# Optimization experiments

Measured on AMD Instinct MI355X. Metric: run time of the kernel, lower is better.

## Reference

```python
import jax, jax.numpy as jnp
import numpy as np

N_NODES = 50000
N_EDGES = 800000
IN_C, HID_C, OUT_C = 128, 64, 40


def setup_inputs() -> dict:
    key = jax.random.key(0)
    ks = jax.random.split(key, 8)
    x = jax.random.normal(ks[0], (N_NODES, IN_C), dtype=jnp.float32)
    edge_index = jax.random.randint(ks[1], (2, N_EDGES), 0, N_NODES, dtype=jnp.int32)
    # Glorot-style init for the three GCNConv linear layers (bias zero as in PyG default reset)
    def glorot(k, fan_in, fan_out):
        lim = jnp.sqrt(6.0 / (fan_in + fan_out)).astype(jnp.float32)
        return jax.random.uniform(k, (fan_in, fan_out), dtype=jnp.float32, minval=-lim, maxval=lim)
    return {
        "x": x,
        "edge_index": edge_index,
        "W1": glorot(ks[2], IN_C, HID_C), "b1": jnp.zeros((HID_C,), jnp.float32),
        "W2": glorot(ks[3], HID_C, HID_C), "b2": jnp.zeros((HID_C,), jnp.float32),
        "W3": glorot(ks[4], HID_C, OUT_C), "b3": jnp.zeros((OUT_C,), jnp.float32),
    }


def _gcn_norm(edge_index, num_nodes):
    # PyG gcn_norm: add self-loops (weight 1), symmetric D^-1/2 (A+I) D^-1/2.
    loop = jnp.arange(num_nodes, dtype=edge_index.dtype)
    row = jnp.concatenate([edge_index[0], loop])  # source
    col = jnp.concatenate([edge_index[1], loop])  # target
    w = jnp.ones(row.shape[0], dtype=jnp.float32)
    deg = jax.ops.segment_sum(w, col, num_segments=num_nodes)
    dinv = jnp.where(deg > 0, jax.lax.rsqrt(deg), 0.0)
    norm = dinv[row] * w * dinv[col]  # [E+N]
    return row, col, norm


def _gcn_conv(x, row, col, norm, W, b):
    h = x @ W                         # linear first, as in PyG GCNConv
    msg = h[row] * norm[:, None]      # gather + scale  [E+N, F]
    agg = jax.ops.segment_sum(msg, col, num_segments=x.shape[0])
    return agg + b


def reference(x, edge_index, W1, b1, W2, b2, W3, b3):
    row, col, norm = _gcn_norm(edge_index, x.shape[0])
    h = jax.nn.relu(_gcn_conv(x, row, col, norm, W1, b1))   # dropout: eval-mode identity
    h = jax.nn.relu(_gcn_conv(h, row, col, norm, W2, b2))
    h = _gcn_conv(h, row, col, norm, W3, b3)
    return jax.nn.log_softmax(h, axis=-1)
```

## Files before the change

### kernel.cpp

```cpp
#include <hip/hip_runtime.h>
#include <hip/hip_bf16.h>
#include <math.h>


#define BSHIFT 10
#define CHUNK 2048
#define CAP 24576

__global__ __launch_bounds__(64) void tinyzero_kernel(int* __restrict__ p) {
  p[threadIdx.x] = 0;
}


__global__ __launch_bounds__(256) void bucketA_kernel(const int* __restrict__ row,
                                                      const int* __restrict__ col,
                                                      int* __restrict__ bcursor,
                                                      int2* __restrict__ tmp, int e) {
  __shared__ int bcnt[64], bstart[64], bbase[64];
  __shared__ int2 stage[CHUNK];
  int tid = threadIdx.x;
  int base = blockIdx.x * CHUNK;
  int cnt = e - base;
  if (cnt > CHUNK) cnt = CHUNK;
  if (tid < 64) bcnt[tid] = 0;
  __syncthreads();

  int2 ed[CHUNK / 256];
  int rk[CHUNK / 256];
#pragma unroll
  for (int k = 0; k < CHUNK / 256; ++k) {
    int j = tid + k * 256;
    if (j < cnt) {
      int c = col[base + j], r = row[base + j];
      ed[k] = make_int2(c, r);
      rk[k] = atomicAdd(&bcnt[c >> BSHIFT], 1);
    }
  }
  __syncthreads();
  if (tid < 64) {
    int v = bcnt[tid];
    int run = v;
#pragma unroll
    for (int off = 1; off < 64; off <<= 1) {
      int t = __shfl_up(run, off);
      if (tid >= off) run += t;
    }
    bstart[tid] = run - v;
    if (v > 0) bbase[tid] = atomicAdd(&bcursor[tid], v);
  }
  __syncthreads();
#pragma unroll
  for (int k = 0; k < CHUNK / 256; ++k) {
    int j = tid + k * 256;
    if (j < cnt) stage[bstart[ed[k].x >> BSHIFT] + rk[k]] = ed[k];
  }
  __syncthreads();
  for (int s = tid; s < cnt; s += 256) {
    int2 ev = stage[s];
    int b = ev.x >> BSHIFT;
    tmp[(size_t)b * CAP + bbase[b] + (s - bstart[b])] = ev;
  }
}


__global__ __launch_bounds__(256) void scatterB_kernel(const int2* __restrict__ tmp,
                                                       const int* __restrict__ bcursor,
                                                       int4* __restrict__ meta,
                                                       float* __restrict__ dinv,
                                                       int* __restrict__ csr, int n) {
  __shared__ int cnt[1 << BSHIFT];
  __shared__ int part[256];
  int tid = threadIdx.x;
  int b = blockIdx.x;
  int node0 = b << BSHIFT;
  int m = bcursor[b];
  const int2* src = tmp + (size_t)b * CAP;

  for (int t = tid; t < (1 << BSHIFT); t += 256) cnt[t] = 0;
  __syncthreads();
  for (int i = tid; i < m; i += 256)
    atomicAdd(&cnt[src[i].x & ((1 << BSHIFT) - 1)], 1);
  __syncthreads();

  int c0 = cnt[tid * 4 + 0], c1 = cnt[tid * 4 + 1];
  int c2 = cnt[tid * 4 + 2], c3 = cnt[tid * 4 + 3];
  int lsum = c0 + c1 + c2 + c3;
  part[tid] = lsum;
  __syncthreads();
#pragma unroll
  for (int off = 1; off < 256; off <<= 1) {
    int t = (tid >= off) ? part[tid - off] : 0;
    __syncthreads();
    part[tid] += t;
    __syncthreads();
  }
  int e0 = (tid == 0 ? 0 : part[tid - 1]);
  int e1 = e0 + c0, e2 = e1 + c1, e3 = e2 + c2;
  int base = b * CAP;

  int nd = node0 + tid * 4;
  if (nd + 0 < n) { float d = rsqrtf((float)(c0 + 1)); meta[nd + 0] = make_int4(base + e0, c0, __float_as_int(d), 0); dinv[nd + 0] = d; }
  if (nd + 1 < n) { float d = rsqrtf((float)(c1 + 1)); meta[nd + 1] = make_int4(base + e1, c1, __float_as_int(d), 0); dinv[nd + 1] = d; }
  if (nd + 2 < n) { float d = rsqrtf((float)(c2 + 1)); meta[nd + 2] = make_int4(base + e2, c2, __float_as_int(d), 0); dinv[nd + 2] = d; }
  if (nd + 3 < n) { float d = rsqrtf((float)(c3 + 1)); meta[nd + 3] = make_int4(base + e3, c3, __float_as_int(d), 0); dinv[nd + 3] = d; }
  __syncthreads();
  cnt[tid * 4 + 0] = e0; cnt[tid * 4 + 1] = e1;
  cnt[tid * 4 + 2] = e2; cnt[tid * 4 + 3] = e3;
  __syncthreads();

  for (int i = tid; i < m; i += 256) {
    int2 ev = src[i];
    int pos = atomicAdd(&cnt[ev.x & ((1 << BSHIFT) - 1)], 1);
    csr[base + pos] = ev.y;
  }
}


template <int K, int F>
__global__ __launch_bounds__(256) void gemm_kernel(const float* __restrict__ X,
                                                   const float* __restrict__ W,
                                                   const float* __restrict__ dinv,
                                                   __hip_bfloat16* __restrict__ Y, int n) {
  __shared__ float xs[16][K];
  int tid = threadIdx.x;
  int node0 = blockIdx.x * 16;
  constexpr int KV = K / 4;
  const float4* X4 = (const float4*)X;
  for (int i = tid; i < 16 * KV; i += 256) {
    int r = i / KV, c = i % KV;
    int nd = node0 + r;
    float4 v = make_float4(0.f, 0.f, 0.f, 0.f);
    if (nd < n) v = X4[(size_t)nd * KV + c];
    ((float4*)&xs[r][0])[c] = v;
  }
  __syncthreads();
  int g = tid >> 6, lane = tid & 63;
  if (lane < F) {
    float acc0 = 0.f, acc1 = 0.f, acc2 = 0.f, acc3 = 0.f;
#pragma unroll 8
    for (int k = 0; k < K; ++k) {
      float w = W[k * F + lane];
      acc0 += xs[g * 4 + 0][k] * w;
      acc1 += xs[g * 4 + 1][k] * w;
      acc2 += xs[g * 4 + 2][k] * w;
      acc3 += xs[g * 4 + 3][k] * w;
    }
    float accs[4] = {acc0, acc1, acc2, acc3};
#pragma unroll
    for (int j = 0; j < 4; ++j) {
      int nd = node0 + g * 4 + j;
      if (nd < n) Y[(size_t)nd * F + lane] = __float2bfloat16(accs[j] * dinv[nd]);
    }
  }
}


__device__ __forceinline__ float bflo(unsigned int u) {
  return __uint_as_float(u << 16);
}
__device__ __forceinline__ float bfhi(unsigned int u) {
  return __uint_as_float(u & 0xffff0000u);
}

template <int F, int MODE>
__global__ __launch_bounds__(256) void agg_kernel(const unsigned short* __restrict__ Hs,
                                                  const int* __restrict__ csr,
                                                  const int4* __restrict__ meta,
                                                  const float* __restrict__ bias,
                                                  float* __restrict__ Y, int n) {
  constexpr int FO = F / 8;
  int wv = (blockIdx.x * 256 + threadIdx.x) >> 6;
  int lane = threadIdx.x & 63;
  int q = lane >> 4;
  int l16 = lane & 15;
  int sub = l16 >> 3;
  int fid = lane & 7;
  int node = wv * 4 + q;
  if (node >= n) return;
  bool activeF = (FO == 8) || (fid < FO);
  int qbase = q * 16;

  int4 mt = meta[node];
  int s = mt.x, e = mt.x + mt.y;
  float di = __int_as_float(mt.z);

  float a0 = 0.f, a1 = 0.f, a2 = 0.f, a3 = 0.f;
  float a4 = 0.f, a5 = 0.f, a6 = 0.f, a7 = 0.f;
  if (sub == 0 && activeF) {
    uint4 u = *(const uint4*)(Hs + (size_t)node * F + 8 * fid);
    a0 = bflo(u.x); a1 = bfhi(u.x); a2 = bflo(u.y); a3 = bfhi(u.y);
    a4 = bflo(u.z); a5 = bfhi(u.z); a6 = bflo(u.w); a7 = bfhi(u.w);
  }

  for (int base = s; base < e; base += 16) {
    int rem = e - base;
    int cnt = rem < 16 ? rem : 16;
    int p = csr[base + (l16 < cnt ? l16 : 0)];
    int j = 0;
    for (; j + 8 <= cnt; j += 8) {
      int r0 = __shfl(p, qbase + j + 0 + sub);
      int r1 = __shfl(p, qbase + j + 2 + sub);
      int r2 = __shfl(p, qbase + j + 4 + sub);
      int r3 = __shfl(p, qbase + j + 6 + sub);
      if (activeF) {
        uint4 u0 = *(const uint4*)(Hs + (size_t)r0 * F + 8 * fid);
        uint4 u1 = *(const uint4*)(Hs + (size_t)r1 * F + 8 * fid);
        uint4 u2 = *(const uint4*)(Hs + (size_t)r2 * F + 8 * fid);
        uint4 u3 = *(const uint4*)(Hs + (size_t)r3 * F + 8 * fid);
        a0 += bflo(u0.x); a1 += bfhi(u0.x); a2 += bflo(u0.y); a3 += bfhi(u0.y);
        a4 += bflo(u0.z); a5 += bfhi(u0.z); a6 += bflo(u0.w); a7 += bfhi(u0.w);
        a0 += bflo(u1.x); a1 += bfhi(u1.x); a2 += bflo(u1.y); a3 += bfhi(u1.y);
        a4 += bflo(u1.z); a5 += bfhi(u1.z); a6 += bflo(u1.w); a7 += bfhi(u1.w);
        a0 += bflo(u2.x); a1 += bfhi(u2.x); a2 += bflo(u2.y); a3 += bfhi(u2.y);
        a4 += bflo(u2.z); a5 += bfhi(u2.z); a6 += bflo(u2.w); a7 += bfhi(u2.w);
        a0 += bflo(u3.x); a1 += bfhi(u3.x); a2 += bflo(u3.y); a3 += bfhi(u3.y);
        a4 += bflo(u3.z); a5 += bfhi(u3.z); a6 += bflo(u3.w); a7 += bfhi(u3.w);
      }
    }
    for (; j < cnt; j += 2) {
      int idx = j + sub;
      int r = __shfl(p, qbase + (idx < cnt ? idx : j));
      if (activeF && idx < cnt) {
        uint4 u = *(const uint4*)(Hs + (size_t)r * F + 8 * fid);
        a0 += bflo(u.x); a1 += bfhi(u.x); a2 += bflo(u.y); a3 += bfhi(u.y);
        a4 += bflo(u.z); a5 += bfhi(u.z); a6 += bflo(u.w); a7 += bfhi(u.w);
      }
    }
  }

  a0 += __shfl_xor(a0, 8);
  a1 += __shfl_xor(a1, 8);
  a2 += __shfl_xor(a2, 8);
  a3 += __shfl_xor(a3, 8);
  a4 += __shfl_xor(a4, 8);
  a5 += __shfl_xor(a5, 8);
  a6 += __shfl_xor(a6, 8);
  a7 += __shfl_xor(a7, 8);

  if (MODE == 0) {
    if (sub == 0 && activeF) {
      float4 b0 = *(const float4*)(bias + 8 * fid);
      float4 b1 = *(const float4*)(bias + 8 * fid + 4);
      float v0 = a0 * di + b0.x, v1 = a1 * di + b0.y;
      float v2 = a2 * di + b0.z, v3 = a3 * di + b0.w;
      float v4 = a4 * di + b1.x, v5 = a5 * di + b1.y;
      float v6 = a6 * di + b1.z, v7 = a7 * di + b1.w;
      v0 = v0 > 0.f ? v0 : 0.f; v1 = v1 > 0.f ? v1 : 0.f;
      v2 = v2 > 0.f ? v2 : 0.f; v3 = v3 > 0.f ? v3 : 0.f;
      v4 = v4 > 0.f ? v4 : 0.f; v5 = v5 > 0.f ? v5 : 0.f;
      v6 = v6 > 0.f ? v6 : 0.f; v7 = v7 > 0.f ? v7 : 0.f;
      float* yp = Y + (size_t)node * F + 8 * fid;
      *(float4*)yp = make_float4(v0, v1, v2, v3);
      *(float4*)(yp + 4) = make_float4(v4, v5, v6, v7);
    }
  } else {
    float v0 = -INFINITY, v1 = -INFINITY, v2 = -INFINITY, v3 = -INFINITY;
    float v4 = -INFINITY, v5 = -INFINITY, v6 = -INFINITY, v7 = -INFINITY;
    if (activeF) {
      float4 b0 = *(const float4*)(bias + 8 * fid);
      float4 b1 = *(const float4*)(bias + 8 * fid + 4);
      v0 = a0 * di + b0.x; v1 = a1 * di + b0.y;
      v2 = a2 * di + b0.z; v3 = a3 * di + b0.w;
      v4 = a4 * di + b1.x; v5 = a5 * di + b1.y;
      v6 = a6 * di + b1.z; v7 = a7 * di + b1.w;
    }
    float m = fmaxf(fmaxf(fmaxf(v0, v1), fmaxf(v2, v3)),
                    fmaxf(fmaxf(v4, v5), fmaxf(v6, v7)));
#pragma unroll
    for (int off = 4; off; off >>= 1) m = fmaxf(m, __shfl_xor(m, off));
    float ex = 0.f;
    if (activeF)
      ex = expf(v0 - m) + expf(v1 - m) + expf(v2 - m) + expf(v3 - m) +
           expf(v4 - m) + expf(v5 - m) + expf(v6 - m) + expf(v7 - m);
#pragma unroll
    for (int off = 4; off; off >>= 1) ex += __shfl_xor(ex, off);
    float lg = m + logf(ex);
    if (sub == 0 && activeF) {
      float* yp = Y + (size_t)node * F + 8 * fid;
      *(float4*)yp = make_float4(v0 - lg, v1 - lg, v2 - lg, v3 - lg);
      *(float4*)(yp + 4) = make_float4(v4 - lg, v5 - lg, v6 - lg, v7 - lg);
    }
  }
}


extern "C" void kernel_launch(void* const* d_in, const int* in_sizes, int n_in,
                              void* d_out, int out_size, void* d_ws, size_t ws_size,
                              hipStream_t stream) {
  const float* x  = (const float*)d_in[0];
  const int*   ei = (const int*)d_in[1];
  const float* W1 = (const float*)d_in[2];
  const float* b1 = (const float*)d_in[3];
  const float* W2 = (const float*)d_in[4];
  const float* b2 = (const float*)d_in[5];
  const float* W3 = (const float*)d_in[6];
  const float* b3 = (const float*)d_in[7];
  float* out = (float*)d_out;

  const int N = in_sizes[0] / 128;
  const int E = in_sizes[1] / 2;
  const int* erow = ei;
  const int* ecol = ei + E;

  const int nbuckets = (N + (1 << BSHIFT) - 1) >> BSHIFT;

  auto align_up = [](size_t v) { return (v + 255) & ~(size_t)255; };
  char* ws = (char*)d_ws;
  size_t off = 0;
  int* bcursor  = (int*)(ws + off); off += align_up(64 * 4);
  int4* meta    = (int4*)(ws + off); off += align_up((size_t)N * 16);
  float* dinv   = (float*)(ws + off); off += align_up((size_t)N * 4);
  int* csr      = (int*)(ws + off); off += align_up((size_t)nbuckets * CAP * 4);
  int2* tmp     = (int2*)(ws + off); off += align_up((size_t)nbuckets * CAP * 8);
  __hip_bfloat16* bufH = (__hip_bfloat16*)(ws + off); off += align_up((size_t)N * 64 * 2);
  float* bufF   = (float*)(ws + off); off += align_up((size_t)N * 64 * 4);
  (void)ws_size;

  const int cb = (E + CHUNK - 1) / CHUNK;

  tinyzero_kernel<<<1, 64, 0, stream>>>(bcursor);
  bucketA_kernel<<<cb, 256, 0, stream>>>(erow, ecol, bcursor, tmp, E);
  scatterB_kernel<<<nbuckets, 256, 0, stream>>>(tmp, bcursor, meta, dinv, csr, N);

  const int gemm_blocks = (N + 15) / 16;
  const int agg_blocks = (N + 15) / 16;

  gemm_kernel<128, 64><<<gemm_blocks, 256, 0, stream>>>(x, W1, dinv, bufH, N);
  agg_kernel<64, 0><<<agg_blocks, 256, 0, stream>>>((const unsigned short*)bufH, csr, meta, b1, bufF, N);

  gemm_kernel<64, 64><<<gemm_blocks, 256, 0, stream>>>(bufF, W2, dinv, bufH, N);
  agg_kernel<64, 0><<<agg_blocks, 256, 0, stream>>>((const unsigned short*)bufH, csr, meta, b2, bufF, N);

  gemm_kernel<64, 40><<<gemm_blocks, 256, 0, stream>>>(bufF, W3, dinv, bufH, N);
  agg_kernel<40, 1><<<agg_blocks, 256, 0, stream>>>((const unsigned short*)bufH, csr, meta, b3, out, N);
}
```

Measured before the change: 165.6 us.

## Pack edges into 32-bit words and store hidden activations as bf16

Edges are packed as a single 32-bit word with the target in the high 16 bits and the source in the low 16 bits, halving temporary bucket traffic. Aggregation outputs for hidden layers are written as bf16 and the following GEMM reads bf16 and expands it to float in shared memory. This cuts memory traffic between stages. The packing assumes node IDs fit in 16 bits, and bf16 storage adds rounding error to intermediate activations.

```diff
diff --git a/kernel.cpp b/kernel.cpp
--- a/kernel.cpp
+++ b/kernel.cpp
@@ -15,9 +15,10 @@
 __global__ __launch_bounds__(256) void bucketA_kernel(const int* __restrict__ row,
                                                       const int* __restrict__ col,
                                                       int* __restrict__ bcursor,
-                                                      int2* __restrict__ tmp, int e) {
+                                                      unsigned int* __restrict__ tmp,
+                                                      int e) {
   __shared__ int bcnt[64], bstart[64], bbase[64];
-  __shared__ int2 stage[CHUNK];
+  __shared__ unsigned int stage[CHUNK];
   int tid = threadIdx.x;
   int base = blockIdx.x * CHUNK;
   int cnt = e - base;
@@ -25,14 +26,14 @@
   if (tid < 64) bcnt[tid] = 0;
   __syncthreads();
 
-  int2 ed[CHUNK / 256];
+  unsigned int ed[CHUNK / 256];
   int rk[CHUNK / 256];
 #pragma unroll
   for (int k = 0; k < CHUNK / 256; ++k) {
     int j = tid + k * 256;
     if (j < cnt) {
       int c = col[base + j], r = row[base + j];
-      ed[k] = make_int2(c, r);
+      ed[k] = ((unsigned int)c << 16) | (unsigned int)r;
       rk[k] = atomicAdd(&bcnt[c >> BSHIFT], 1);
     }
   }
@@ -52,18 +53,18 @@
 #pragma unroll
   for (int k = 0; k < CHUNK / 256; ++k) {
     int j = tid + k * 256;
-    if (j < cnt) stage[bstart[ed[k].x >> BSHIFT] + rk[k]] = ed[k];
+    if (j < cnt) stage[bstart[ed[k] >> (16 + BSHIFT)] + rk[k]] = ed[k];
   }
   __syncthreads();
   for (int s = tid; s < cnt; s += 256) {
-    int2 ev = stage[s];
-    int b = ev.x >> BSHIFT;
+    unsigned int ev = stage[s];
+    int b = ev >> (16 + BSHIFT);
     tmp[(size_t)b * CAP + bbase[b] + (s - bstart[b])] = ev;
   }
 }
 
 
-__global__ __launch_bounds__(256) void scatterB_kernel(const int2* __restrict__ tmp,
+__global__ __launch_bounds__(256) void scatterB_kernel(const unsigned int* __restrict__ tmp,
                                                        const int* __restrict__ bcursor,
                                                        int4* __restrict__ meta,
                                                        float* __restrict__ dinv,
@@ -74,12 +75,12 @@
   int b = blockIdx.x;
   int node0 = b << BSHIFT;
   int m = bcursor[b];
-  const int2* src = tmp + (size_t)b * CAP;
+  const unsigned int* src = tmp + (size_t)b * CAP;
 
   for (int t = tid; t < (1 << BSHIFT); t += 256) cnt[t] = 0;
   __syncthreads();
   for (int i = tid; i < m; i += 256)
-    atomicAdd(&cnt[src[i].x & ((1 << BSHIFT) - 1)], 1);
+    atomicAdd(&cnt[(src[i] >> 16) & ((1 << BSHIFT) - 1)], 1);
   __syncthreads();
 
   int c0 = cnt[tid * 4 + 0], c1 = cnt[tid * 4 + 1];
@@ -109,29 +110,57 @@
   __syncthreads();
 
   for (int i = tid; i < m; i += 256) {
-    int2 ev = src[i];
-    int pos = atomicAdd(&cnt[ev.x & ((1 << BSHIFT) - 1)], 1);
-    csr[base + pos] = ev.y;
-  }
-}
-
-
-template <int K, int F>
-__global__ __launch_bounds__(256) void gemm_kernel(const float* __restrict__ X,
+    unsigned int ev = src[i];
+    int pos = atomicAdd(&cnt[(ev >> 16) & ((1 << BSHIFT) - 1)], 1);
+    csr[base + pos] = (int)(ev & 0xFFFFu);
+  }
+}
+
+
+__device__ __forceinline__ float bflo(unsigned int u) {
+  return __uint_as_float(u << 16);
+}
+__device__ __forceinline__ float bfhi(unsigned int u) {
+  return __uint_as_float(u & 0xffff0000u);
+}
+__device__ __forceinline__ unsigned int pack2bf(float a, float b) {
+  __hip_bfloat16 ha = __float2bfloat16(a), hb = __float2bfloat16(b);
+  unsigned short ua = *(unsigned short*)&ha, ub = *(unsigned short*)&hb;
+  return (unsigned int)ua | ((unsigned int)ub << 16);
+}
+
+
+template <int K, int F, bool BF16IN>
+__global__ __launch_bounds__(256) void gemm_kernel(const void* __restrict__ Xv,
                                                    const float* __restrict__ W,
                                                    const float* __restrict__ dinv,
                                                    __hip_bfloat16* __restrict__ Y, int n) {
   __shared__ float xs[16][K];
   int tid = threadIdx.x;
   int node0 = blockIdx.x * 16;
-  constexpr int KV = K / 4;
-  const float4* X4 = (const float4*)X;
-  for (int i = tid; i < 16 * KV; i += 256) {
-    int r = i / KV, c = i % KV;
-    int nd = node0 + r;
-    float4 v = make_float4(0.f, 0.f, 0.f, 0.f);
-    if (nd < n) v = X4[(size_t)nd * KV + c];
-    ((float4*)&xs[r][0])[c] = v;
+  if (BF16IN) {
+    constexpr int KV = K / 8;
+    const uint4* X4 = (const uint4*)Xv;
+    for (int i = tid; i < 16 * KV; i += 256) {
+      int r = i / KV, c = i % KV;
+      int nd = node0 + r;
+      uint4 v = make_uint4(0u, 0u, 0u, 0u);
+      if (nd < n) v = X4[(size_t)nd * KV + c];
+      float4 lo = make_float4(bflo(v.x), bfhi(v.x), bflo(v.y), bfhi(v.y));
+      float4 hi = make_float4(bflo(v.z), bfhi(v.z), bflo(v.w), bfhi(v.w));
+      ((float4*)&xs[r][0])[c * 2] = lo;
+      ((float4*)&xs[r][0])[c * 2 + 1] = hi;
+    }
+  } else {
+    constexpr int KV = K / 4;
+    const float4* X4 = (const float4*)Xv;
+    for (int i = tid; i < 16 * KV; i += 256) {
+      int r = i / KV, c = i % KV;
+      int nd = node0 + r;
+      float4 v = make_float4(0.f, 0.f, 0.f, 0.f);
+      if (nd < n) v = X4[(size_t)nd * KV + c];
+      ((float4*)&xs[r][0])[c] = v;
+    }
   }
   __syncthreads();
   int g = tid >> 6, lane = tid & 63;
@@ -155,19 +184,12 @@
 }
 
 
-__device__ __forceinline__ float bflo(unsigned int u) {
-  return __uint_as_float(u << 16);
-}
-__device__ __forceinline__ float bfhi(unsigned int u) {
-  return __uint_as_float(u & 0xffff0000u);
-}
-
 template <int F, int MODE>
 __global__ __launch_bounds__(256) void agg_kernel(const unsigned short* __restrict__ Hs,
                                                   const int* __restrict__ csr,
                                                   const int4* __restrict__ meta,
                                                   const float* __restrict__ bias,
-                                                  float* __restrict__ Y, int n) {
+                                                  void* __restrict__ Yout, int n) {
   constexpr int FO = F / 8;
   int wv = (blockIdx.x * 256 + threadIdx.x) >> 6;
   int lane = threadIdx.x & 63;
@@ -249,9 +271,10 @@
       v2 = v2 > 0.f ? v2 : 0.f; v3 = v3 > 0.f ? v3 : 0.f;
       v4 = v4 > 0.f ? v4 : 0.f; v5 = v5 > 0.f ? v5 : 0.f;
       v6 = v6 > 0.f ? v6 : 0.f; v7 = v7 > 0.f ? v7 : 0.f;
-      float* yp = Y + (size_t)node * F + 8 * fid;
-      *(float4*)yp = make_float4(v0, v1, v2, v3);
-      *(float4*)(yp + 4) = make_float4(v4, v5, v6, v7);
+      uint4 o;
+      o.x = pack2bf(v0, v1); o.y = pack2bf(v2, v3);
+      o.z = pack2bf(v4, v5); o.w = pack2bf(v6, v7);
+      *(uint4*)((unsigned short*)Yout + (size_t)node * F + 8 * fid) = o;
     }
   } else {
     float v0 = -INFINITY, v1 = -INFINITY, v2 = -INFINITY, v3 = -INFINITY;
@@ -276,7 +299,7 @@
     for (int off = 4; off; off >>= 1) ex += __shfl_xor(ex, off);
     float lg = m + logf(ex);
     if (sub == 0 && activeF) {
-      float* yp = Y + (size_t)node * F + 8 * fid;
+      float* yp = (float*)Yout + (size_t)node * F + 8 * fid;
       *(float4*)yp = make_float4(v0 - lg, v1 - lg, v2 - lg, v3 - lg);
       *(float4*)(yp + 4) = make_float4(v4 - lg, v5 - lg, v6 - lg, v7 - lg);
     }
@@ -311,9 +334,9 @@
   int4* meta    = (int4*)(ws + off); off += align_up((size_t)N * 16);
   float* dinv   = (float*)(ws + off); off += align_up((size_t)N * 4);
   int* csr      = (int*)(ws + off); off += align_up((size_t)nbuckets * CAP * 4);
-  int2* tmp     = (int2*)(ws + off); off += align_up((size_t)nbuckets * CAP * 8);
+  unsigned int* tmp = (unsigned int*)(ws + off); off += align_up((size_t)nbuckets * CAP * 4);
   __hip_bfloat16* bufH = (__hip_bfloat16*)(ws + off); off += align_up((size_t)N * 64 * 2);
-  float* bufF   = (float*)(ws + off); off += align_up((size_t)N * 64 * 4);
+  __hip_bfloat16* bufA = (__hip_bfloat16*)(ws + off); off += align_up((size_t)N * 64 * 2);
   (void)ws_size;
 
   const int cb = (E + CHUNK - 1) / CHUNK;
@@ -325,12 +348,12 @@
   const int gemm_blocks = (N + 15) / 16;
   const int agg_blocks = (N + 15) / 16;
 
-  gemm_kernel<128, 64><<<gemm_blocks, 256, 0, stream>>>(x, W1, dinv, bufH, N);
-  agg_kernel<64, 0><<<agg_blocks, 256, 0, stream>>>((const unsigned short*)bufH, csr, meta, b1, bufF, N);
-
-  gemm_kernel<64, 64><<<gemm_blocks, 256, 0, stream>>>(bufF, W2, dinv, bufH, N);
-  agg_kernel<64, 0><<<agg_blocks, 256, 0, stream>>>((const unsigned short*)bufH, csr, meta, b2, bufF, N);
-
-  gemm_kernel<64, 40><<<gemm_blocks, 256, 0, stream>>>(bufF, W3, dinv, bufH, N);
+  gemm_kernel<128, 64, false><<<gemm_blocks, 256, 0, stream>>>(x, W1, dinv, bufH, N);
+  agg_kernel<64, 0><<<agg_blocks, 256, 0, stream>>>((const unsigned short*)bufH, csr, meta, b1, bufA, N);
+
+  gemm_kernel<64, 64, true><<<gemm_blocks, 256, 0, stream>>>(bufA, W2, dinv, bufH, N);
+  agg_kernel<64, 0><<<agg_blocks, 256, 0, stream>>>((const unsigned short*)bufH, csr, meta, b2, bufA, N);
+
+  gemm_kernel<64, 40, true><<<gemm_blocks, 256, 0, stream>>>(bufA, W3, dinv, bufH, N);
   agg_kernel<40, 1><<<agg_blocks, 256, 0, stream>>>((const unsigned short*)bufH, csr, meta, b3, out, N);
 }
```

After: 165.6 us. About the same (-0.0%).
